# Kernel optimization log

Hardware: AMD Instinct MI355X
Metric: run time of the kernel (lower is better)

## Reference

```python
import jax, jax.numpy as jnp
import numpy as np

G = 64  # voxel grid extent per axis; grid_ind entries are in [0, G)


def setup_inputs() -> dict:
    key = jax.random.key(0)
    k1, k2 = jax.random.split(key)
    N = 4_000_000
    points = jax.random.normal(k1, (N, 7), dtype=jnp.float32)
    grid_ind = jax.random.randint(k2, (N, 3), 0, G, dtype=jnp.int64)
    return {"points": points, "grid_ind": grid_ind}


def reference(points, grid_ind):
    # torch.unique(grid_ind, dim=0, return_inverse=True) sorts rows
    # lexicographically; for nonnegative coords that equals sorting the
    # linearized index, so we dedup the linear id instead of rows.
    N = points.shape[0]
    gi = grid_ind.astype(jnp.int32)
    lin = (gi[:, 0] * G + gi[:, 1]) * G + gi[:, 2]  # [N]
    # fixed-size unique for jit compatibility: at most N unique voxels,
    # padded with fill_value=-1 at the tail.
    unq, unq_inv = jnp.unique(lin, return_inverse=True, size=N, fill_value=-1)
    # scatter_mean over point->voxel mapping
    sums = jax.ops.segment_sum(points, unq_inv, num_segments=N)          # [N, 7]
    cnt = jax.ops.segment_sum(jnp.ones((N,), points.dtype), unq_inv,
                              num_segments=N)                            # [N]
    mean = sums / jnp.maximum(cnt, 1.0)[:, None]
    # reconstruct the [n_unique_padded, 3] voxel coordinates (pad rows = -1)
    valid = unq >= 0
    u = jnp.maximum(unq, 0)
    unq3 = jnp.stack([u // (G * G), (u // G) % G, u % G], axis=-1)
    unq3 = jnp.where(valid[:, None], unq3, -1).astype(grid_ind.dtype)
    return mean, unq3
```

## Files before the change

### kernel.cpp

```cpp
#include <hip/hip_runtime.h>

#define NVOX 262144
#define NB   256
#define NREP 8
#define VPB  1024
#define PPB  4096
#define SCT  1024
#define CHK  4096
#define NBLK 256

__global__ void dv_fill(const unsigned* __restrict__ nuP,
                        float* __restrict__ out, int n) {
    int nu = (int)*nuP;
    size_t meanChunks = (size_t)n * 7 / 4;
    size_t coordChunks = (size_t)n * 3 / 4;
    size_t total = meanChunks + coordChunks;
    size_t i = (size_t)blockIdx.x * blockDim.x + threadIdx.x;
    if (i >= total) return;
    float* mean = out;
    float* coords = out + (size_t)n * 7;
    if (i < meanChunks) {
        size_t base = i * 4, lim = (size_t)nu * 7;
        if (base >= lim) {
            *(float4*)(mean + base) = make_float4(0.f, 0.f, 0.f, 0.f);
        } else if (base + 4 > lim) {
            for (size_t k = lim; k < base + 4; ++k) mean[k] = 0.f;
        }
    } else {
        size_t base = (i - meanChunks) * 4, lim = (size_t)nu * 3;
        if (base >= lim) {
            *(float4*)(coords + base) = make_float4(-1.f, -1.f, -1.f, -1.f);
        } else if (base + 4 > lim) {
            for (size_t k = lim; k < base + 4; ++k) coords[k] = -1.f;
        }
    }
}

__device__ __forceinline__ unsigned bf16rne(float x) {
    unsigned u = __float_as_uint(x);
    u += 0x7fffu + ((u >> 16) & 1u);
    return u >> 16;
}

__global__ void __launch_bounds__(SCT) rx_scatfuse(
        const int* __restrict__ gi, const float* __restrict__ pts, int n,
        unsigned* __restrict__ cursor, int capb, int capb8,
        uint4* __restrict__ recs) {
    __shared__ uint4 recS[PPB];
    __shared__ unsigned short bkS[PPB];
    __shared__ unsigned hist[NB];
    __shared__ unsigned bStart[NB];
    __shared__ unsigned combo[NB];
    __shared__ unsigned wsumS[8];
    int t = threadIdx.x, b = blockIdx.x;
    int lane = t & 63, wid = t >> 6;
    unsigned rep = (unsigned)(b & (NREP - 1));
    int base = b * PPB;
    int cnt = n - base;
    if (cnt > PPB) cnt = PPB;
    if (t < NB) hist[t] = 0;
    __syncthreads();

    unsigned keyA[PPB / SCT], rankA[PPB / SCT];
    float f[28];
    int p0 = base + t * 4;
    bool full = (p0 + 4 <= n);
    if (full) {
        const int4* g4 = (const int4*)(gi + (size_t)base * 3);
        int4 a = g4[3 * t], c = g4[3 * t + 1], d = g4[3 * t + 2];
        const float4* p4 = (const float4*)(pts + (size_t)base * 7) +
                           (size_t)t * 7;
        float4 u0 = p4[0], u1 = p4[1], u2 = p4[2], u3 = p4[3];
        float4 u4 = p4[4], u5 = p4[5], u6 = p4[6];
        keyA[0] = ((unsigned)((a.x << 2) | (a.y >> 4)) << 10) |
                  (unsigned)(((a.y & 15) << 6) | a.z);
        keyA[1] = ((unsigned)((a.w << 2) | (c.x >> 4)) << 10) |
                  (unsigned)(((c.x & 15) << 6) | c.y);
        keyA[2] = ((unsigned)((c.z << 2) | (c.w >> 4)) << 10) |
                  (unsigned)(((c.w & 15) << 6) | d.x);
        keyA[3] = ((unsigned)((d.y << 2) | (d.z >> 4)) << 10) |
                  (unsigned)(((d.z & 15) << 6) | d.w);
#pragma unroll
        for (int j = 0; j < 4; ++j)
            rankA[j] = atomicAdd(&hist[keyA[j] >> 10], 1u);
        f[0] = u0.x; f[1] = u0.y; f[2] = u0.z; f[3] = u0.w;
        f[4] = u1.x; f[5] = u1.y; f[6] = u1.z; f[7] = u1.w;
        f[8] = u2.x; f[9] = u2.y; f[10] = u2.z; f[11] = u2.w;
        f[12] = u3.x; f[13] = u3.y; f[14] = u3.z; f[15] = u3.w;
        f[16] = u4.x; f[17] = u4.y; f[18] = u4.z; f[19] = u4.w;
        f[20] = u5.x; f[21] = u5.y; f[22] = u5.z; f[23] = u5.w;
        f[24] = u6.x; f[25] = u6.y; f[26] = u6.z; f[27] = u6.w;
    } else {
#pragma unroll
        for (int j = 0; j < 4; ++j) {
            int i = p0 + j;
            if (i < n) {
                int g0 = gi[3 * i], g1 = gi[3 * i + 1], g2 = gi[3 * i + 2];
                keyA[j] = ((unsigned)((g0 << 2) | (g1 >> 4)) << 10) |
                          (unsigned)(((g1 & 15) << 6) | g2);
                rankA[j] = atomicAdd(&hist[keyA[j] >> 10], 1u);
            }
        }
    }
    __syncthreads();
    unsigned mine = (t < NB) ? hist[t] : 0u;
    unsigned x = mine;
#pragma unroll
    for (int d = 1; d < 64; d <<= 1) {
        unsigned y = __shfl_up(x, d, 64);
        if (lane >= d) x += y;
    }
    if (t < NB && lane == 63) wsumS[wid] = x;
    __syncthreads();
    if (t < 64) {
        unsigned w = (lane < 4) ? wsumS[lane] : 0u, xx = w;
#pragma unroll
        for (int d = 1; d < 4; d <<= 1) {
            unsigned y = __shfl_up(xx, d, 64);
            if (lane >= d) xx += y;
        }
        if (lane < 4) wsumS[lane] = xx - w;
    }
    __syncthreads();
    if (t < NB) {
        unsigned incl = x + wsumS[wid];
        unsigned bs = incl - mine;
        bStart[t] = bs;
        unsigned rs = (mine > 0)
            ? atomicAdd(&cursor[rep * NB + (unsigned)t], mine) : 0u;
        combo[t] = (unsigned)t * (unsigned)capb + rep * (unsigned)capb8 +
                   rs - bs;
    }
    __syncthreads();

    if (full) {
#pragma unroll
        for (int j = 0; j < 4; ++j) {
            unsigned key = keyA[j], rank = rankA[j];
            unsigned bk = key >> 10, sub = key & 1023u;
            uint4 r;
            r.x = bf16rne(f[j * 7 + 0]) | (bf16rne(f[j * 7 + 1]) << 16);
            r.y = bf16rne(f[j * 7 + 2]) | (bf16rne(f[j * 7 + 3]) << 16);
            r.z = bf16rne(f[j * 7 + 4]) | (bf16rne(f[j * 7 + 5]) << 16);
            r.w = bf16rne(f[j * 7 + 6]) | (sub << 16);
            unsigned sp = bStart[bk] + rank;
            recS[sp] = r;
            bkS[sp] = (unsigned short)bk;
        }
    } else {
#pragma unroll
        for (int j = 0; j < 4; ++j) {
            int lid = t * 4 + j;
            if (lid < cnt) {
                int i = base + lid;
                const float* p = pts + (size_t)i * 7;
                float f0 = p[0], f1 = p[1], f2 = p[2], f3 = p[3];
                float f4 = p[4], f5 = p[5], f6 = p[6];
                unsigned key = keyA[j], rank = rankA[j];
                unsigned bk = key >> 10, sub = key & 1023u;
                uint4 r;
                r.x = bf16rne(f0) | (bf16rne(f1) << 16);
                r.y = bf16rne(f2) | (bf16rne(f3) << 16);
                r.z = bf16rne(f4) | (bf16rne(f5) << 16);
                r.w = bf16rne(f6) | (sub << 16);
                unsigned sp = bStart[bk] + rank;
                recS[sp] = r;
                bkS[sp] = (unsigned short)bk;
            }
        }
    }
    __syncthreads();
#pragma unroll
    for (int k = 0; k < PPB / SCT; ++k) {
        int j = k * SCT + t;
        if (j < cnt) {
            unsigned bk = bkS[j];
            recs[combo[bk] + (unsigned)j] = recS[j];
        }
    }
}

__global__ void __launch_bounds__(1024) rx_accum(
        const uint4* __restrict__ recs, const unsigned* __restrict__ cursor,
        int capb8, float* __restrict__ accTable,
        unsigned* __restrict__ occCount) {
    __shared__ uint4 sortedR[CHK];
    __shared__ unsigned cnt_[VPB];
    __shared__ unsigned wsum[16];
    int t = threadIdx.x, bk = blockIdx.x;
    int lane = t & 63, wid = t >> 6;
    unsigned pre[9];
    pre[0] = 0;
#pragma unroll
    for (int r_ = 0; r_ < NREP; ++r_)
        pre[r_ + 1] = pre[r_] + cursor[r_ * NB + bk];
    unsigned len = pre[NREP];
    size_t base = (size_t)bk * (unsigned)(capb8 * NREP);
    unsigned c8 = (unsigned)capb8;

    auto MAP = [&](unsigned idx) -> size_t {
        unsigned seg = 0, p = 0;
#pragma unroll
        for (int q = 1; q < NREP; ++q)
            if (idx >= pre[q]) { seg = (unsigned)q; p = pre[q]; }
        return base + (size_t)seg * c8 + (idx - p);
    };

    float a0 = 0.f, a1 = 0.f, a2 = 0.f, a3 = 0.f,
          a4 = 0.f, a5 = 0.f, a6 = 0.f, cf = 0.f;

    bool v[4]; uint4 r[4];
    bool vn[4]; uint4 rn[4];
#pragma unroll
    for (int j = 0; j < 4; ++j) {
        unsigned idx = (unsigned)(j * 1024) + t;
        v[j] = idx < len;
        if (v[j]) r[j] = recs[MAP(idx)];
    }

    for (unsigned cs = 0; cs < len; cs += CHK) {
        cnt_[t] = 0;
        __syncthreads();
        unsigned k[4], rk[4];
#pragma unroll
        for (int j = 0; j < 4; ++j)
            if (v[j]) {
                k[j] = r[j].w >> 16;
                rk[j] = atomicAdd(&cnt_[k[j]], 1u);
            }
        __syncthreads();
        unsigned own = cnt_[t];
        unsigned x = own;
#pragma unroll
        for (int d = 1; d < 64; d <<= 1) {
            unsigned y = __shfl_up(x, d, 64);
            if (lane >= d) x += y;
        }
        if (lane == 63) wsum[wid] = x;
        __syncthreads();
        if (t < 64) {
            unsigned w = (lane < 16) ? wsum[lane] : 0u;
            unsigned xx = w;
#pragma unroll
            for (int d = 1; d < 16; d <<= 1) {
                unsigned y = __shfl_up(xx, d, 64);
                if (lane >= d) xx += y;
            }
            if (lane < 16) wsum[lane] = xx - w;
        }
        __syncthreads();
        unsigned excl = x - own + wsum[wid];
        cnt_[t] = excl;
        __syncthreads();
#pragma unroll
        for (int j = 0; j < 4; ++j)
            if (v[j]) sortedR[cnt_[k[j]] + rk[j]] = r[j];
        unsigned ns = cs + CHK;
        if (ns < len) {
#pragma unroll
            for (int j = 0; j < 4; ++j) {
                unsigned idx = ns + (unsigned)(j * 1024) + t;
                vn[j] = idx < len;
                if (vn[j]) rn[j] = recs[MAP(idx)];
            }
        }
        __syncthreads();
        unsigned st = excl, end = excl + own;
        for (unsigned q = st; q < end; ++q) {
            uint4 rr = sortedR[q];
            a0 += __uint_as_float(rr.x << 16);
            a1 += __uint_as_float(rr.x & 0xffff0000u);
            a2 += __uint_as_float(rr.y << 16);
            a3 += __uint_as_float(rr.y & 0xffff0000u);
            a4 += __uint_as_float(rr.z << 16);
            a5 += __uint_as_float(rr.z & 0xffff0000u);
            a6 += __uint_as_float(rr.w << 16);
            cf += 1.f;
        }
        if (ns < len) {
#pragma unroll
            for (int j = 0; j < 4; ++j) { v[j] = vn[j]; if (vn[j]) r[j] = rn[j]; }
        }
    }
    float4* o = (float4*)(accTable + ((size_t)bk * VPB + t) * 8);
    o[0] = make_float4(a0, a1, a2, a3);
    o[1] = make_float4(a4, a5, a6, cf);
    unsigned long long m = __ballot(cf > 0.f);
    if (lane == 0) wsum[wid] = (unsigned)__popcll(m);
    __syncthreads();
    if (t == 0) {
        unsigned occ = 0;
#pragma unroll
        for (int w = 0; w < 16; ++w) occ += wsum[w];
        occCount[bk] = occ;
    }
}

__global__ void __launch_bounds__(1024) rx_emit(
        const float* __restrict__ accTable,
        const unsigned* __restrict__ occCount,
        float* __restrict__ out_mean, float* __restrict__ out_coords,
        int n) {
    int bk = blockIdx.x, t = threadIdx.x;
    int lane = t & 63, wid = t >> 6;
    __shared__ unsigned wsB[4];
    __shared__ unsigned wsum[16];
    __shared__ unsigned rankBaseS, nuS;

    unsigned mineB = 0, xB = 0;
    if (t < NB) {
        mineB = occCount[t];
        xB = mineB;
#pragma unroll
        for (int d = 1; d < 64; d <<= 1) {
            unsigned y = __shfl_up(xB, d, 64);
            if (lane >= d) xB += y;
        }
        if (lane == 63) wsB[wid] = xB;
    }
    __syncthreads();
    if (t < 64) {
        unsigned w = (lane < 4) ? wsB[lane] : 0u, xx = w;
#pragma unroll
        for (int d = 1; d < 4; d <<= 1) {
            unsigned y = __shfl_up(xx, d, 64);
            if (lane >= d) xx += y;
        }
        if (lane < 4) wsB[lane] = xx - w;
    }
    __syncthreads();
    if (t < NB) {
        unsigned incl = xB + wsB[wid];
        if (t == bk) rankBaseS = incl - mineB;
        if (t == NB - 1) nuS = incl;
    }
    __syncthreads();

    const float4* a = (const float4*)(accTable + ((size_t)bk * VPB + t) * 8);
    float4 r0 = a[0], r1 = a[1];
    unsigned flag = (r1.w > 0.f) ? 1u : 0u;
    unsigned x = flag;
#pragma unroll
    for (int d = 1; d < 64; d <<= 1) {
        unsigned y = __shfl_up(x, d, 64);
        if (lane >= d) x += y;
    }
    if (lane == 63) wsum[wid] = x;
    __syncthreads();
    if (t < 64) {
        unsigned w = (lane < 16) ? wsum[lane] : 0u, xx = w;
#pragma unroll
        for (int d = 1; d < 16; d <<= 1) {
            unsigned y = __shfl_up(xx, d, 64);
            if (lane >= d) xx += y;
        }
        if (lane < 16) wsum[lane] = xx - w;
    }
    __syncthreads();
    unsigned excl = x - flag + wsum[wid];
    if (flag) {
        int r = (int)(rankBaseS + excl);
        int lin = (bk << 10) | t;
        float inv = 1.0f / r1.w;
        float* m = out_mean + (size_t)r * 7;
        m[0] = r0.x * inv; m[1] = r0.y * inv; m[2] = r0.z * inv;
        m[3] = r0.w * inv; m[4] = r1.x * inv; m[5] = r1.y * inv;
        m[6] = r1.z * inv;
        float* cd = out_coords + (size_t)r * 3;
        cd[0] = (float)(lin >> 12);
        cd[1] = (float)((lin >> 6) & 63);
        cd[2] = (float)(lin & 63);
    }

    int nu = (int)nuS;
    size_t meanChunks = (size_t)n * 7 / 4;
    size_t coordChunks = (size_t)n * 3 / 4;
    size_t total = meanChunks + coordChunks;
    size_t stride = (size_t)gridDim.x * blockDim.x;
    float* mean = out_mean;
    float* coords = out_mean + (size_t)n * 7;
    for (size_t i = (size_t)bk * blockDim.x + t; i < total; i += stride) {
        if (i < meanChunks) {
            size_t base = i * 4, lim = (size_t)nu * 7;
            if (base >= lim) {
                *(float4*)(mean + base) = make_float4(0.f, 0.f, 0.f, 0.f);
            } else if (base + 4 > lim) {
                for (size_t k = lim; k < base + 4; ++k) mean[k] = 0.f;
            }
        } else {
            size_t base = (i - meanChunks) * 4, lim = (size_t)nu * 3;
            if (base >= lim) {
                *(float4*)(coords + base) = make_float4(-1.f, -1.f, -1.f, -1.f);
            } else if (base + 4 > lim) {
                for (size_t k = lim; k < base + 4; ++k) coords[k] = -1.f;
            }
        }
    }
}

struct Meta {
    unsigned blockSums[NBLK];
    unsigned blockFlagSums[NBLK];
    unsigned blockOffs[NBLK];
    unsigned blockRankOffs[NBLK];
    unsigned nUnique;
};

__global__ void dv_count(const int* __restrict__ gi, int n,
                         unsigned* __restrict__ counts,
                         unsigned short* __restrict__ slots) {
    int i = blockIdx.x * blockDim.x + threadIdx.x;
    if (i >= n) return;
    int lin = (gi[3 * i] << 12) | (gi[3 * i + 1] << 6) | gi[3 * i + 2];
    unsigned s = atomicAdd(&counts[lin], 1u);
    slots[i] = (unsigned short)s;
}

__global__ void dv_bs1(const unsigned* __restrict__ counts,
                       Meta* __restrict__ meta) {
    int b = blockIdx.x, t = threadIdx.x;
    uint4 c = ((const uint4*)(counts + (size_t)b * 1024))[t];
    unsigned cs = c.x + c.y + c.z + c.w;
    unsigned fs = (c.x > 0) + (c.y > 0) + (c.z > 0) + (c.w > 0);
    __shared__ unsigned smC[256], smF[256];
    smC[t] = cs; smF[t] = fs;
    __syncthreads();
    for (int off = 128; off > 0; off >>= 1) {
        if (t < off) { smC[t] += smC[t + off]; smF[t] += smF[t + off]; }
        __syncthreads();
    }
    if (t == 0) { meta->blockSums[b] = smC[0]; meta->blockFlagSums[b] = smF[0]; }
}

__global__ void dv_scan2(unsigned* __restrict__ offsets, int n,
                         Meta* __restrict__ meta) {
    __shared__ unsigned smC[NBLK], smF[NBLK];
    int t = threadIdx.x;
    unsigned c = meta->blockSums[t], f = meta->blockFlagSums[t];
    smC[t] = c; smF[t] = f;
    __syncthreads();
    for (int off = 1; off < NBLK; off <<= 1) {
        unsigned vc = (t >= off) ? smC[t - off] : 0u;
        unsigned vf = (t >= off) ? smF[t - off] : 0u;
        __syncthreads();
        smC[t] += vc; smF[t] += vf;
        __syncthreads();
    }
    meta->blockOffs[t] = smC[t] - c;
    meta->blockRankOffs[t] = smF[t] - f;
    if (t == NBLK - 1) { meta->nUnique = smF[t]; offsets[NVOX] = (unsigned)n; }
}

__global__ void dv_scan3(unsigned* __restrict__ counts,
                         const Meta* __restrict__ meta) {
    int b = blockIdx.x, t = threadIdx.x;
    uint4 c = ((const uint4*)(counts + (size_t)b * 1024))[t];
    unsigned mysum = c.x + c.y + c.z + c.w;
    __shared__ unsigned sm[256];
    sm[t] = mysum;
    __syncthreads();
    for (int off = 1; off < 256; off <<= 1) {
        unsigned v = (t >= off) ? sm[t - off] : 0u;
        __syncthreads();
        sm[t] += v;
        __syncthreads();
    }
    unsigned base = meta->blockOffs[b] + sm[t] - mysum;
    uint4 o;
    o.x = base;
    o.y = base + c.x;
    o.z = o.y + c.y;
    o.w = o.z + c.z;
    ((uint4*)(counts + (size_t)b * 1024))[t] = o;
}

__global__ void dv_scatter2(const int* __restrict__ gi, int n,
                            const unsigned* __restrict__ offsets,
                            const unsigned short* __restrict__ slots,
                            unsigned* __restrict__ perm) {
    int i = blockIdx.x * blockDim.x + threadIdx.x;
    if (i >= n) return;
    int lin = (gi[3 * i] << 12) | (gi[3 * i + 1] << 6) | gi[3 * i + 2];
    perm[offsets[lin] + (unsigned)slots[i]] = (unsigned)i;
}

__global__ void dv_emit2(const float* __restrict__ points,
                         const unsigned* __restrict__ offsets,
                         const unsigned* __restrict__ perm,
                         const Meta* __restrict__ meta,
                         float* __restrict__ out_mean,
                         float* __restrict__ out_coords) {
    int b = blockIdx.x, t = threadIdx.x;
    int base = b * 1024 + t * 4;
    uint4 o4 = ((const uint4*)offsets)[b * 256 + t];
    unsigned o[5];
    o[0] = o4.x; o[1] = o4.y; o[2] = o4.z; o[3] = o4.w;
    o[4] = offsets[base + 4];
    int c[4], pre[4], mycount = 0;
#pragma unroll
    for (int j = 0; j < 4; ++j) {
        c[j] = (int)(o[j + 1] - o[j]);
        pre[j] = mycount;
        mycount += (c[j] > 0) ? 1 : 0;
    }
    __shared__ int sm[256];
    sm[t] = mycount;
    __syncthreads();
    for (int off = 1; off < 256; off <<= 1) {
        int v = (t >= off) ? sm[t - off] : 0;
        __syncthreads();
        sm[t] += v;
        __syncthreads();
    }
    int rank0 = (int)meta->blockRankOffs[b] + (sm[t] - mycount);
#pragma unroll
    for (int j = 0; j < 4; ++j) {
        if (c[j] > 0) {
            float s0 = 0.f, s1 = 0.f, s2 = 0.f, s3 = 0.f,
                  s4 = 0.f, s5 = 0.f, s6 = 0.f;
            for (unsigned k = o[j]; k < o[j + 1]; ++k) {
                unsigned idx = perm[k];
                const float* p = points + (size_t)idx * 7;
                s0 += p[0]; s1 += p[1]; s2 += p[2]; s3 += p[3];
                s4 += p[4]; s5 += p[5]; s6 += p[6];
            }
            int r = rank0 + pre[j];
            int v = base + j;
            float inv = 1.0f / (float)c[j];
            float* m = out_mean + (size_t)r * 7;
            m[0] = s0 * inv; m[1] = s1 * inv; m[2] = s2 * inv;
            m[3] = s3 * inv; m[4] = s4 * inv; m[5] = s5 * inv;
            m[6] = s6 * inv;
            float* cd = out_coords + (size_t)r * 3;
            cd[0] = (float)(v >> 12);
            cd[1] = (float)((v >> 6) & 63);
            cd[2] = (float)(v & 63);
        }
    }
}

extern "C" void kernel_launch(void* const* d_in, const int* in_sizes, int n_in,
                              void* d_out, int out_size, void* d_ws, size_t ws_size,
                              hipStream_t stream) {
    const float* points = (const float*)d_in[0];
    const int*   gi     = (const int*)d_in[1];
    int n = in_sizes[0] / 7;

    float* out_mean   = (float*)d_out;
    float* out_coords = (float*)d_out + (size_t)n * 7;

    int threads = 256;
    int nb1 = (n + PPB - 1) / PPB;

    int capb8 = (n / NB + n / NB / 8 + 1024) / NREP;
    int capb  = capb8 * NREP;
    size_t recsB = (size_t)NB * capb * 16;
    size_t accB  = (size_t)NB * VPB * 8 * sizeof(float);
    size_t need  = recsB + accB + (size_t)NB * NREP * 4  +
                   NB * 4  + 256;

    size_t fillChunks = (size_t)n * 7 / 4 + (size_t)n * 3 / 4;
    int fillBlocks = (int)((fillChunks + threads - 1) / threads);

    if (ws_size >= need) {
        char* w = (char*)d_ws;
        uint4*    recs     = (uint4*)w;                    w += recsB;
        float*    accTable = (float*)w;                    w += accB;
        unsigned* cursor   = (unsigned*)w;                 w += (size_t)NB * NREP * 4;
        unsigned* occCount = (unsigned*)w;

        hipMemsetAsync(cursor, 0, (size_t)NB * NREP * 4, stream);
        rx_scatfuse<<<nb1, SCT, 0, stream>>>(gi, points, n, cursor, capb,
                                             capb8, recs);
        rx_accum<<<NB, 1024, 0, stream>>>(recs, cursor, capb8, accTable,
                                          occCount);
        rx_emit<<<NB, 1024, 0, stream>>>(accTable, occCount, out_mean,
                                         out_coords, n);
    } else {
        char* w = (char*)d_ws;
        unsigned*       perm    = (unsigned*)w;
        unsigned short* slots   = (unsigned short*)(w + (size_t)n * 4);
        unsigned*       offsets = (unsigned*)(w + (size_t)n * 4 + (size_t)n * 2);
        Meta*           meta    = (Meta*)((char*)offsets + (size_t)(NVOX + 4) * 4);

        hipMemsetAsync(offsets, 0, (size_t)(NVOX + 4) * 4, stream);

        int blocksN = (n + threads - 1) / threads;
        dv_count<<<blocksN, threads, 0, stream>>>(gi, n, offsets, slots);
        dv_bs1<<<NBLK, 256, 0, stream>>>(offsets, meta);
        dv_scan2<<<1, NBLK, 0, stream>>>(offsets, n, meta);
        dv_scan3<<<NBLK, 256, 0, stream>>>(offsets, meta);
        dv_scatter2<<<blocksN, threads, 0, stream>>>(gi, n, offsets, slots, perm);
        dv_emit2<<<NBLK, 256, 0, stream>>>(points, offsets, perm, meta,
                                           out_mean, out_coords);
        dv_fill<<<fillBlocks, threads, 0, stream>>>(&meta->nUnique,
                                                    (float*)d_out, n);
    }
}
```

Baseline: 348.7 us.

## Move output padding fill from emit kernel into scatter kernel

The full-output default fill (zeros for the means, -1 for the coordinates) now runs as a grid-stride loop at the end of the scatter kernel, and rx_emit's tail-fill loop is removed. The emit kernel later overwrites the valid rows. The intent is to take the large fill write out of the small 256-block emit kernel, spread it over the wide scatter grid, and overlap it with scatter work. In exchange the whole output is written, not only the tail beyond the unique count, so more bytes go to memory. Correctness depends on rx_emit running after rx_scatfuse on the same stream.

```diff
diff --git a/kernel.cpp b/kernel.cpp
--- a/kernel.cpp
+++ b/kernel.cpp
@@ -45,7 +45,7 @@
 __global__ void __launch_bounds__(SCT) rx_scatfuse(
         const int* __restrict__ gi, const float* __restrict__ pts, int n,
         unsigned* __restrict__ cursor, int capb, int capb8,
-        uint4* __restrict__ recs) {
+        uint4* __restrict__ recs, float* __restrict__ outFill) {
     __shared__ uint4 recS[PPB];
     __shared__ unsigned short bkS[PPB];
     __shared__ unsigned hist[NB];
@@ -178,6 +178,19 @@
             recs[combo[bk] + (unsigned)j] = recS[j];
         }
     }
+
+    {
+        float4* o4p = (float4*)outFill;
+        size_t meanChunks = (size_t)n * 7 / 4;
+        size_t totalChunks = meanChunks + (size_t)n * 3 / 4;
+        const float4 z4 = make_float4(0.f, 0.f, 0.f, 0.f);
+        const float4 m4 = make_float4(-1.f, -1.f, -1.f, -1.f);
+        size_t stride = (size_t)gridDim.x * SCT;
+        for (size_t i = (size_t)b * SCT + (size_t)t; i < totalChunks;
+             i += stride) {
+            o4p[i] = (i < meanChunks) ? z4 : m4;
+        }
+    }
 }
 
 __global__ void __launch_bounds__(1024) rx_accum(
@@ -299,13 +312,12 @@
 __global__ void __launch_bounds__(1024) rx_emit(
         const float* __restrict__ accTable,
         const unsigned* __restrict__ occCount,
-        float* __restrict__ out_mean, float* __restrict__ out_coords,
-        int n) {
+        float* __restrict__ out_mean, float* __restrict__ out_coords) {
     int bk = blockIdx.x, t = threadIdx.x;
     int lane = t & 63, wid = t >> 6;
     __shared__ unsigned wsB[4];
     __shared__ unsigned wsum[16];
-    __shared__ unsigned rankBaseS, nuS;
+    __shared__ unsigned rankBaseS;
 
     unsigned mineB = 0, xB = 0;
     if (t < NB) {
@@ -332,7 +344,6 @@
     if (t < NB) {
         unsigned incl = xB + wsB[wid];
         if (t == bk) rankBaseS = incl - mineB;
-        if (t == NB - 1) nuS = incl;
     }
     __syncthreads();
 
@@ -370,31 +381,6 @@
         cd[0] = (float)(lin >> 12);
         cd[1] = (float)((lin >> 6) & 63);
         cd[2] = (float)(lin & 63);
-    }
-
-    int nu = (int)nuS;
-    size_t meanChunks = (size_t)n * 7 / 4;
-    size_t coordChunks = (size_t)n * 3 / 4;
-    size_t total = meanChunks + coordChunks;
-    size_t stride = (size_t)gridDim.x * blockDim.x;
-    float* mean = out_mean;
-    float* coords = out_mean + (size_t)n * 7;
-    for (size_t i = (size_t)bk * blockDim.x + t; i < total; i += stride) {
-        if (i < meanChunks) {
-            size_t base = i * 4, lim = (size_t)nu * 7;
-            if (base >= lim) {
-                *(float4*)(mean + base) = make_float4(0.f, 0.f, 0.f, 0.f);
-            } else if (base + 4 > lim) {
-                for (size_t k = lim; k < base + 4; ++k) mean[k] = 0.f;
-            }
-        } else {
-            size_t base = (i - meanChunks) * 4, lim = (size_t)nu * 3;
-            if (base >= lim) {
-                *(float4*)(coords + base) = make_float4(-1.f, -1.f, -1.f, -1.f);
-            } else if (base + 4 > lim) {
-                for (size_t k = lim; k < base + 4; ++k) coords[k] = -1.f;
-            }
-        }
     }
 }
 
@@ -571,11 +557,11 @@
 
         hipMemsetAsync(cursor, 0, (size_t)NB * NREP * 4, stream);
         rx_scatfuse<<<nb1, SCT, 0, stream>>>(gi, points, n, cursor, capb,
-                                             capb8, recs);
+                                             capb8, recs, (float*)d_out);
         rx_accum<<<NB, 1024, 0, stream>>>(recs, cursor, capb8, accTable,
                                           occCount);
         rx_emit<<<NB, 1024, 0, stream>>>(accTable, occCount, out_mean,
-                                         out_coords, n);
+                                         out_coords);
     } else {
         char* w = (char*)d_ws;
         unsigned*       perm    = (unsigned*)w;
```

New measurement: 370.4 us. 6.2% more time.
